# Optimization experiments

Hardware: AMD Instinct MI355X
Metric: run time of the kernel (lower is better)

The kernel has to match this reference:

```python
import jax, jax.numpy as jnp
import numpy as np


def _ln(x, g, b):
    m = x.mean(-1, keepdims=True)
    v = ((x - m) ** 2).mean(-1, keepdims=True)
    return (x - m) * jax.lax.rsqrt(v + 1e-5) * g + b


def _forward(x, fx_in, pre_w1, pre_b1, pre_w2, pre_b2, placeholder,
             ln1_g, ln1_b, px_w, px_b, pfx_w, pfx_b, slice_w, slice_b, temp,
             q_w, k_w, v_w, out_w, out_b, ln2_g, ln2_b,
             mlp_w1, mlp_b1, mlp_w2, mlp_b2,
             ln3_g, ln3_b, head_w1, head_b1, head_w2, head_b2):
    # All linear weights are stored as [in, out] (pre-transposed vs torch nn.Linear).
    B, N, _ = x.shape
    L, H = temp.shape
    dh = slice_w.shape[1]
    gelu = lambda t: jax.nn.gelu(t, approximate=False)
    # preprocess MLP (n_layers=0, res=False): Linear -> GELU -> Linear
    h = jnp.concatenate([x, fx_in], axis=-1)
    h = gelu(h @ pre_w1 + pre_b1) @ pre_w2 + pre_b2
    h = h + placeholder  # learned [D] offset
    scale = 1.0 / jnp.sqrt(jnp.asarray(dh, h.dtype))
    for i in range(L):  # loop over structurally distinct layers
        y = _ln(h, ln1_g[i], ln1_b[i])
        # project to per-head features: bhnd
        fx_mid = (y @ pfx_w[i] + pfx_b[i]).reshape(B, N, H, dh).transpose(0, 2, 1, 3)
        x_mid = (y @ px_w[i] + px_b[i]).reshape(B, N, H, dh).transpose(0, 2, 1, 3)
        # soft slice assignment over G slices
        logits = jnp.einsum('bhnd,dg->bhng', x_mid, slice_w[i]) + slice_b[i]
        sw = jax.nn.softmax(logits / temp[i][None, :, None, None], axis=-1)  # bhng
        norm = sw.sum(axis=2)  # bhg
        tok = jnp.einsum('bhnd,bhng->bhgd', fx_mid, sw) / (norm + 1e-5)[..., None]
        # attention over G=slice_num tokens
        q = tok @ q_w[i]
        k = tok @ k_w[i]
        v = tok @ v_w[i]
        attn = jax.nn.softmax(jnp.einsum('bhgd,bhmd->bhgm', q, k) * scale, axis=-1)
        out_slice = jnp.einsum('bhgm,bhmd->bhgd', attn, v)
        # deslice back to points
        out_x = jnp.einsum('bhgd,bhng->bhnd', out_slice, sw)
        out_x = out_x.transpose(0, 2, 1, 3).reshape(B, N, H * dh)
        h = h + (out_x @ out_w[i] + out_b[i])
        z = _ln(h, ln2_g[i], ln2_b[i])
        h = h + (gelu(z @ mlp_w1[i] + mlp_b1[i]) @ mlp_w2[i] + mlp_b2[i])
    z = _ln(h, ln3_g, ln3_b)
    return gelu(z @ head_w1 + head_b1) @ head_w2 + head_b2


def setup_inputs() -> dict:
    key = jax.random.key(0)
    B, N, D, H, dh, G, L = 2, 16384, 256, 8, 32, 64, 5
    SP, FUN, OUT = 2, 4, 4
    ID = H * dh  # inner_dim == n_hidden
    MR = D * 1   # mlp_ratio=1
    ks = iter(jax.random.split(key, 64))
    nrm = lambda shape, s=0.02: jax.random.normal(next(ks), shape, jnp.float32) * s
    return dict(
        x=jax.random.normal(next(ks), (B, N, SP), jnp.float32),
        fx_in=jax.random.normal(next(ks), (B, N, FUN), jnp.float32),
        pre_w1=nrm((SP + FUN, 2 * D)), pre_b1=jnp.zeros((2 * D,), jnp.float32),
        pre_w2=nrm((2 * D, D)), pre_b2=jnp.zeros((D,), jnp.float32),
        placeholder=nrm((D,)),
        ln1_g=jnp.ones((L, D), jnp.float32), ln1_b=jnp.zeros((L, D), jnp.float32),
        px_w=nrm((L, D, ID)), px_b=jnp.zeros((L, ID), jnp.float32),
        pfx_w=nrm((L, D, ID)), pfx_b=jnp.zeros((L, ID), jnp.float32),
        slice_w=nrm((L, dh, G), 0.1), slice_b=jnp.zeros((L, G), jnp.float32),
        temp=0.5 * jnp.ones((L, H), jnp.float32),
        q_w=nrm((L, dh, dh), 0.1), k_w=nrm((L, dh, dh), 0.1), v_w=nrm((L, dh, dh), 0.1),
        out_w=nrm((L, ID, D)), out_b=jnp.zeros((L, D), jnp.float32),
        ln2_g=jnp.ones((L, D), jnp.float32), ln2_b=jnp.zeros((L, D), jnp.float32),
        mlp_w1=nrm((L, D, MR)), mlp_b1=jnp.zeros((L, MR), jnp.float32),
        mlp_w2=nrm((L, MR, D)), mlp_b2=jnp.zeros((L, D), jnp.float32),
        ln3_g=jnp.ones((D,), jnp.float32), ln3_b=jnp.zeros((D,), jnp.float32),
        head_w1=nrm((D, D)), head_b1=jnp.zeros((D,), jnp.float32),
        head_w2=nrm((D, OUT)), head_b2=jnp.zeros((OUT,), jnp.float32),
    )


def reference(x, fx_in, pre_w1, pre_b1, pre_w2, pre_b2, placeholder,
              ln1_g, ln1_b, px_w, px_b, pfx_w, pfx_b, slice_w, slice_b, temp,
              q_w, k_w, v_w, out_w, out_b, ln2_g, ln2_b,
              mlp_w1, mlp_b1, mlp_w2, mlp_b2,
              ln3_g, ln3_b, head_w1, head_b1, head_w2, head_b2):
    return _forward(x, fx_in, pre_w1, pre_b1, pre_w2, pre_b2, placeholder,
                    ln1_g, ln1_b, px_w, px_b, pfx_w, pfx_b, slice_w, slice_b, temp,
                    q_w, k_w, v_w, out_w, out_b, ln2_g, ln2_b,
                    mlp_w1, mlp_b1, mlp_w2, mlp_b2,
                    ln3_g, ln3_b, head_w1, head_b1, head_w2, head_b2)
```

## Files before the change

### kernel.cpp

```cpp
#include <hip/hip_runtime.h>


#define MTOK 32768
#define NB   16384

typedef unsigned short u16;
using short8 = __attribute__((ext_vector_type(8))) short;
using f4     = __attribute__((ext_vector_type(4))) float;

__device__ __forceinline__ float bfu(u16 u) {
    return __uint_as_float(((unsigned)u) << 16);
}
__device__ __forceinline__ u16 f2bf(float f) {
    unsigned u = __float_as_uint(f);
    u += 0x7FFFu + ((u >> 16) & 1u);
    return (u16)(u >> 16);
}
__device__ __forceinline__ float ldf(const void* p, int i, int isbf) {
    return isbf ? bfu(((const u16*)p)[i]) : ((const float*)p)[i];
}
__device__ __forceinline__ float4 dec4(ushort4 u) {
    return make_float4(bfu(u.x), bfu(u.y), bfu(u.z), bfu(u.w));
}
__device__ __forceinline__ float gelu_f(float x) {
    return 0.5f * x * (1.0f + erff(x * 0.7071067811865475f));
}

typedef __attribute__((address_space(1))) const unsigned int* as1p;
typedef __attribute__((address_space(3))) unsigned int* as3p;
__device__ __forceinline__ void gload_lds16(const u16* g, u16* l) {
    __builtin_amdgcn_global_load_lds((as1p)g, (as3p)l, 16, 0, 0);
}

#define F_H      ((size_t)0)
#define F_OS     ((size_t)8388608)
#define F_TOKP   ((size_t)8421376)
#define F_NORMP  ((size_t)10518528)
#define F_TOK    ((size_t)10584064)
#define F_NORM   ((size_t)10616832)
#define F_BIAS   ((size_t)10617856)
#define F_PARAMS ((size_t)10626048)
#define F_BF     ((size_t)10858884)
#define B_PB2C 0
#define B_OUTB 256
#define B_M1B  1536
#define B_M2B  2816
#define B_HB1  4096
#define B_SP   4352
#define B_END  8192
#define U_WT     ((size_t)0)
#define WT_PRE2  0
#define WT_HEAD1 131072
#define WT_SPFX  196608
#define WT_OUT   1179648
#define WT_MLP1  1507328
#define WT_MLP2  1835008
#define WT_END   2162688
#define U_Y   ((size_t)2162688)
#define U_XM  ((size_t)10551296)
#define U_FM  ((size_t)18939904)
#define U_SW  ((size_t)27328512)

#define P_X    0
#define P_FX   65536
#define P_W1   196608
#define P_B1   199680
#define P_LN1G 200192
#define P_LN1B 201472
#define P_LN2G 202752
#define P_LN2B 204032
#define P_LN3G 205312
#define P_LN3B 205568
#define P_SLW  205824
#define P_SLB  216064
#define P_TEMP 216384
#define P_QW   216448
#define P_KW   221568
#define P_VW   226688
#define P_HW2  231808
#define P_HB2  232832
#define P_END  232836

__global__ __launch_bounds__(256) void cvt_kernel(
    const void* x, const void* fx, const void* w1, const void* b1,
    const void* l1g, const void* l1b, const void* l2g, const void* l2b,
    const void* l3g, const void* l3b, const void* slw, const void* slb,
    const void* tmp, const void* qw, const void* kw, const void* vw,
    const void* hw2, const void* hb2, float* __restrict__ P)
{
    int isbf = (((const u16*)tmp)[0] != 0);
    int idx = blockIdx.x * 256 + threadIdx.x;
    const void* s; int o;
    if      (idx < 65536)  { s = x;   o = idx; }
    else if (idx < 196608) { s = fx;  o = idx - 65536; }
    else if (idx < 199680) { s = w1;  o = idx - 196608; }
    else if (idx < 200192) { s = b1;  o = idx - 199680; }
    else if (idx < 201472) { s = l1g; o = idx - 200192; }
    else if (idx < 202752) { s = l1b; o = idx - 201472; }
    else if (idx < 204032) { s = l2g; o = idx - 202752; }
    else if (idx < 205312) { s = l2b; o = idx - 204032; }
    else if (idx < 205568) { s = l3g; o = idx - 205312; }
    else if (idx < 205824) { s = l3b; o = idx - 205568; }
    else if (idx < 216064) { s = slw; o = idx - 205824; }
    else if (idx < 216384) { s = slb; o = idx - 216064; }
    else if (idx < 216424) { s = tmp; o = idx - 216384; }
    else if (idx < 216448) { return; }
    else if (idx < 221568) { s = qw;  o = idx - 216448; }
    else if (idx < 226688) { s = kw;  o = idx - 221568; }
    else if (idx < 231808) { s = vw;  o = idx - 226688; }
    else if (idx < 232832) { s = hw2; o = idx - 231808; }
    else if (idx < 232836) { s = hb2; o = idx - 232832; }
    else return;
    P[idx] = ldf(s, o, isbf);
}

__global__ __launch_bounds__(256) void prep_main(
    const void* pre_w2, const void* head_w1, const void* pfx_w,
    const void* out_w, const void* mlp_w1, const void* mlp_w2,
    const void* pre_b2, const void* placeholder, const void* pfx_b,
    const void* out_b, const void* mlp_b1, const void* mlp_b2,
    const void* head_b1, const void* tmp,
    u16* __restrict__ WT, float* __restrict__ BIAS)
{
    int isbf = (((const u16*)tmp)[0] != 0);
    int blk = blockIdx.x;
    int t = threadIdx.x;
    if (blk < 368) {
        __shared__ float tile[64][65];
        const void* src; size_t srcoff; size_t dbase; int dstride;
        int k0, n0;
        if (blk < 32) {
            int tk = blk >> 2, tn = blk & 3;
            src = pre_w2; srcoff = 0;
            k0 = tk * 64; n0 = tn * 64;
            dbase = WT_PRE2; dstride = 512;
        } else {
            int m = (blk - 32) >> 4, tl = (blk - 32) & 15;
            int tk = tl >> 2, tn = tl & 3;
            k0 = tk * 64; n0 = tn * 64; dstride = 256;
            if (m == 0)       { src = head_w1; srcoff = 0;               dbase = WT_HEAD1; }
            else if (m <= 5)  { int i = m - 1;  src = pfx_w;  srcoff = (size_t)i * 65536;
                                dbase = WT_SPFX + (size_t)i * 196608 + (size_t)512 * 256; }
            else if (m <= 10) { int i = m - 6;  src = out_w;  srcoff = (size_t)i * 65536;
                                dbase = WT_OUT + (size_t)i * 65536; }
            else if (m <= 15) { int i = m - 11; src = mlp_w1; srcoff = (size_t)i * 65536;
                                dbase = WT_MLP1 + (size_t)i * 65536; }
            else              { int i = m - 16; src = mlp_w2; srcoff = (size_t)i * 65536;
                                dbase = WT_MLP2 + (size_t)i * 65536; }
        }
#pragma unroll
        for (int p = 0; p < 16; ++p) {
            int flat = t + 256 * p;
            int r = flat >> 6, c = flat & 63;
            tile[r][c] = ldf(src, srcoff + (size_t)(k0 + r) * 256 + n0 + c, isbf);
        }
        __syncthreads();
#pragma unroll
        for (int p = 0; p < 16; ++p) {
            int flat = t + 256 * p;
            int r = flat >> 6, c = flat & 63;
            WT[dbase + (size_t)(n0 + r) * dstride + k0 + c] = f2bf(tile[c][r]);
        }
    } else {
        int idx = (blk - 368) * 256 + t;
        if (idx < 256) {
            BIAS[B_PB2C + idx] = ldf(pre_b2, idx, isbf) + ldf(placeholder, idx, isbf);
        } else if (idx < 1536) {
            int o = idx - 256;  BIAS[B_OUTB + o] = ldf(out_b, o, isbf);
        } else if (idx < 2816) {
            int o = idx - 1536; BIAS[B_M1B + o] = ldf(mlp_b1, o, isbf);
        } else if (idx < 4096) {
            int o = idx - 2816; BIAS[B_M2B + o] = ldf(mlp_b2, o, isbf);
        } else if (idx < 4352) {
            int o = idx - 4096; BIAS[B_HB1 + o] = ldf(head_b1, o, isbf);
        } else if (idx < 5632) {
            int o = idx - 4352;
            int i = o >> 8, c = o & 255;
            BIAS[B_SP + i * 768 + 512 + c] = ldf(pfx_b, o, isbf);
        }
    }
}

__global__ __launch_bounds__(256) void prep_pxsl(
    const void* px_w, const void* px_b, const void* slw, const void* slb,
    const void* tmp, u16* __restrict__ WT, float* __restrict__ BIAS)
{
    int isbf = (((const u16*)tmp)[0] != 0);
    __shared__ float pxs[64 * 33];
    __shared__ float sls[2048];
    int blk = blockIdx.x;
    int i = blk >> 5, h = (blk >> 2) & 7, kb = blk & 3;
    int t = threadIdx.x;
#pragma unroll
    for (int p = 0; p < 8; ++p) {
        int flat = t + 256 * p;
        sls[flat] = ldf(slw, i * 2048 + flat, isbf);
        int k = flat >> 5, d = flat & 31;
        pxs[k * 33 + d] = ldf(px_w, i * 65536 + (kb * 64 + k) * 256 + h * 32 + d, isbf);
    }
    __syncthreads();
    int k = t & 63, gb = t >> 6;
    float acc[16];
#pragma unroll
    for (int gi = 0; gi < 16; ++gi) acc[gi] = 0.f;
#pragma unroll
    for (int d = 0; d < 32; ++d) {
        float pv = pxs[k * 33 + d];
        const float* sp = sls + d * 64 + gb * 16;
#pragma unroll
        for (int gi = 0; gi < 16; ++gi) acc[gi] = fmaf(pv, sp[gi], acc[gi]);
    }
    u16* WTp = WT + WT_SPFX + (size_t)i * 196608;
#pragma unroll
    for (int gi = 0; gi < 16; ++gi) {
        int n = h * 64 + gb * 16 + gi;
        WTp[n * 256 + kb * 64 + k] = f2bf(acc[gi]);
    }
    if (kb == 0 && t < 64) {
        int g = t;
        float a = ldf(slb, i * 64 + g, isbf);
#pragma unroll
        for (int d = 0; d < 32; ++d)
            a = fmaf(ldf(px_b, i * 256 + h * 32 + d, isbf), sls[d * 64 + g], a);
        BIAS[B_SP + i * 768 + h * 64 + g] = a;
    }
}

__global__ __launch_bounds__(256) void pre1_kernel(
    const float* __restrict__ P, u16* __restrict__ HID)
{
    __shared__ float w1s[3072];
    __shared__ float b1s[512];
    int t = threadIdx.x;
#pragma unroll
    for (int p = 0; p < 12; ++p) w1s[t + 256 * p] = P[P_W1 + t + 256 * p];
    b1s[t] = P[P_B1 + t];
    b1s[t + 256] = P[P_B1 + t + 256];
    __syncthreads();
    int m = blockIdx.x * 4 + (t >> 6);
    int lane = t & 63;
    float xa = P[P_X + m * 2],      xb = P[P_X + m * 2 + 1];
    float fa = P[P_FX + m * 4],     fb = P[P_FX + m * 4 + 1];
    float fc = P[P_FX + m * 4 + 2], fd = P[P_FX + m * 4 + 3];
    size_t base = (size_t)m * 512 + lane;
#pragma unroll
    for (int jj = 0; jj < 8; ++jj) {
        int j = lane + 64 * jj;
        float a = b1s[j];
        a = fmaf(xa, w1s[j], a);
        a = fmaf(xb, w1s[512 + j], a);
        a = fmaf(fa, w1s[1024 + j], a);
        a = fmaf(fb, w1s[1536 + j], a);
        a = fmaf(fc, w1s[2048 + j], a);
        a = fmaf(fd, w1s[2560 + j], a);
        HID[base + 64 * jj] = f2bf(gelu_f(a));
    }
}

template <int KK, bool RES>
__global__ __launch_bounds__(256, 3) void gemm_ln(
    const u16* __restrict__ A, const u16* __restrict__ Wt,
    const float* __restrict__ bias, const float* __restrict__ lng,
    const float* __restrict__ lnb, u16* __restrict__ Hb, u16* __restrict__ Y)
{
    __shared__ u16 As[64 * 64];
    __shared__ u16 Bs[256 * 64];
    __shared__ float rs2[2][64], rq2[2][64];
    const int t = threadIdx.x;
    const int wave = t >> 6, lane = t & 63;
    const int quad = lane >> 4, l15 = lane & 15;
    const int m0 = blockIdx.x * 64;
    const int wm = (wave & 1) * 32, wn = (wave >> 1) * 128;
    const int lrow = lane >> 3, ls = lane & 7;
    f4 acc[2][8];
#pragma unroll
    for (int i = 0; i < 2; ++i)
#pragma unroll
        for (int j = 0; j < 8; ++j) acc[i][j] = (f4){0.f, 0.f, 0.f, 0.f};

    for (int kc = 0; kc < KK; kc += 64) {
        if (kc) __syncthreads();
#pragma unroll
        for (int q = 0; q < 10; ++q) {
            int gr = wave * 80 + q * 8;
            if (gr < 64) {
                int row = gr + lrow;
                int chunk = ls ^ lrow;
                gload_lds16(A + (size_t)(m0 + row) * KK + kc + chunk * 8,
                            As + gr * 64);
            } else {
                int brow = gr - 64 + lrow;
                int chunk = ls ^ lrow;
                gload_lds16(Wt + (size_t)brow * KK + kc + chunk * 8,
                            Bs + (gr - 64) * 64);
            }
        }
        __syncthreads();
#pragma unroll
        for (int kk = 0; kk < 2; ++kk) {
            short8 a[2], b[8];
#pragma unroll
            for (int i = 0; i < 2; ++i) {
                int R = wm + i * 16 + l15;
                a[i] = *(const short8*)(As + R * 64 + (((quad + kk * 4) ^ (R & 7)) << 3));
            }
#pragma unroll
            for (int j = 0; j < 8; ++j) {
// ... 132 lines not shown
            }
    }
#pragma unroll
    for (int i = 0; i < 2; ++i)
#pragma unroll
        for (int j = 0; j < 8; ++j) acc[i][j] = (f4){0.f, 0.f, 0.f, 0.f};

    for (int kc = 0; kc < 256; kc += 64) {
        __syncthreads();
#pragma unroll
        for (int q = 0; q < 8; ++q) {
            int gr = wave * 64 + q * 8;
            int brow = gr + lrow;
            gload_lds16(W2 + (size_t)brow * 256 + kc + (ls ^ lrow) * 8,
                        Bs + gr * 64);
        }
        __syncthreads();
#pragma unroll
        for (int kk = 0; kk < 2; ++kk) {
            short8 a[2], b[8];
#pragma unroll
            for (int i = 0; i < 2; ++i) {
                int R = wm + i * 16 + l15;
                a[i] = *(const short8*)(hs + R * 264 + kc + kk * 32 + quad * 8);
            }
#pragma unroll
            for (int j = 0; j < 8; ++j) {
                int Rb = wn + j * 16 + l15;
                b[j] = *(const short8*)(Bs + Rb * 64 + (((quad + kk * 4) ^ (Rb & 7)) << 3));
            }
#pragma unroll
            for (int i = 0; i < 2; ++i)
#pragma unroll
                for (int j = 0; j < 8; ++j)
                    acc[i][j] = __builtin_amdgcn_mfma_f32_16x16x32_bf16(
                        a[i], b[j], acc[i][j], 0, 0, 0);
        }
    }
    float bj[8];
#pragma unroll
    for (int j = 0; j < 8; ++j) bj[j] = b2[colj[j]];
    const int half = wn >> 7;
#pragma unroll
    for (int i = 0; i < 2; ++i) {
#pragma unroll
        for (int r = 0; r < 4; ++r) {
            int row = wm + i * 16 + quad * 4 + r;
            size_t gbase = (size_t)(m0 + row) * 256;
            float s = 0.f, q2 = 0.f;
#pragma unroll
            for (int j = 0; j < 8; ++j) {
                float v = acc[i][j][r] + bj[j] + bfu(Hb[gbase + colj[j]]);
                Hb[gbase + colj[j]] = f2bf(v);
                acc[i][j][r] = v;
                s += v; q2 += v * v;
            }
#pragma unroll
            for (int o = 1; o < 16; o <<= 1) { s += __shfl_xor(s, o); q2 += __shfl_xor(q2, o); }
            if (l15 == 0) { rs2[half][row] = s; rq2[half][row] = q2; }
        }
    }
    __syncthreads();
    float gj[8], betj[8];
#pragma unroll
    for (int j = 0; j < 8; ++j) { gj[j] = lng[colj[j]]; betj[j] = lnb[colj[j]]; }
#pragma unroll
    for (int i = 0; i < 2; ++i) {
#pragma unroll
        for (int r = 0; r < 4; ++r) {
            int row = wm + i * 16 + quad * 4 + r;
            size_t gbase = (size_t)(m0 + row) * 256;
            float mean = (rs2[0][row] + rs2[1][row]) * (1.0f / 256.0f);
            float var = (rq2[0][row] + rq2[1][row]) * (1.0f / 256.0f) - mean * mean;
            float rstd = rsqrtf(var + 1e-5f);
#pragma unroll
            for (int j = 0; j < 8; ++j) {
                float y = (acc[i][j][r] - mean) * rstd * gj[j] + betj[j];
                Y[gbase + colj[j]] = f2bf(y);
            }
        }
    }
}

__global__ __launch_bounds__(256, 4) void gemm_gelu(
    const u16* __restrict__ A, const u16* __restrict__ Wt,
    const float* __restrict__ bias, u16* __restrict__ Cb)
{
    __shared__ u16 As[128 * 64];
    __shared__ u16 Bs[128 * 64];
    const int t = threadIdx.x;
    const int wave = t >> 6, lane = t & 63;
    const int quad = lane >> 4, l15 = lane & 15;
    const int m0 = blockIdx.x * 128;
    const int n0 = blockIdx.y * 128;
    const int wm = (wave & 1) * 64, wn = (wave >> 1) * 64;
    const int r0 = wave * 32;
    const int lrow = lane >> 3, ls = lane & 7;
    f4 acc[4][4];
#pragma unroll
    for (int i = 0; i < 4; ++i)
#pragma unroll
        for (int j = 0; j < 4; ++j) acc[i][j] = (f4){0.f, 0.f, 0.f, 0.f};

    for (int kc = 0; kc < 256; kc += 64) {
        if (kc) __syncthreads();
#pragma unroll
        for (int q = 0; q < 4; ++q) {
            int row = r0 + q * 8 + lrow;
            int chunk = ls ^ (row & 7);
            gload_lds16(A  + (size_t)(m0 + row) * 256 + kc + chunk * 8,
                        As + (r0 + q * 8) * 64);
            gload_lds16(Wt + (size_t)(n0 + row) * 256 + kc + chunk * 8,
                        Bs + (r0 + q * 8) * 64);
        }
        __syncthreads();
#pragma unroll
        for (int kk = 0; kk < 2; ++kk) {
            short8 a[4], b[4];
#pragma unroll
            for (int i = 0; i < 4; ++i) {
                int R = wm + i * 16 + l15;
                a[i] = *(const short8*)(As + R * 64 + (((quad + kk * 4) ^ (R & 7)) << 3));
            }
#pragma unroll
            for (int j = 0; j < 4; ++j) {
                int R = wn + j * 16 + l15;
                b[j] = *(const short8*)(Bs + R * 64 + (((quad + kk * 4) ^ (R & 7)) << 3));
            }
#pragma unroll
            for (int i = 0; i < 4; ++i)
#pragma unroll
                for (int j = 0; j < 4; ++j)
                    acc[i][j] = __builtin_amdgcn_mfma_f32_16x16x32_bf16(
                        a[i], b[j], acc[i][j], 0, 0, 0);
        }
    }
#pragma unroll
    for (int j = 0; j < 4; ++j) {
        int cj = n0 + wn + j * 16 + l15;
        float bj = bias[cj];
#pragma unroll
        for (int i = 0; i < 4; ++i) {
            int rbase = m0 + wm + i * 16 + quad * 4;
#pragma unroll
            for (int r = 0; r < 4; ++r) {
                float v = gelu_f(acc[i][j][r] + bj);
                Cb[(size_t)(rbase + r) * 256 + cj] = f2bf(v);
            }
        }
    }
}

__global__ __launch_bounds__(256, 4) void gemm_spfx(
    const u16* __restrict__ A, const u16* __restrict__ Wt,
    const float* __restrict__ bsp, const float* __restrict__ tempv,
    u16* __restrict__ SW, u16* __restrict__ FM)
{
    __shared__ u16 As[128 * 64];
    __shared__ u16 Bs[128 * 64];
    const int t = threadIdx.x;
    const int wave = t >> 6, lane = t & 63;
    const int quad = lane >> 4, l15 = lane & 15;
    const int m0 = blockIdx.x * 128;
    const int n0 = blockIdx.y * 128;
    const int wm = (wave & 1) * 64, wn = (wave >> 1) * 64;
    const int r0 = wave * 32;
    const int lrow = lane >> 3, ls = lane & 7;
    f4 acc[4][4];
#pragma unroll
    for (int i = 0; i < 4; ++i)
#pragma unroll
        for (int j = 0; j < 4; ++j) acc[i][j] = (f4){0.f, 0.f, 0.f, 0.f};

    for (int kc = 0; kc < 256; kc += 64) {
        if (kc) __syncthreads();
#pragma unroll
        for (int q = 0; q < 4; ++q) {
            int row = r0 + q * 8 + lrow;
            int chunk = ls ^ (row & 7);
            gload_lds16(A  + (size_t)(m0 + row) * 256 + kc + chunk * 8,
                        As + (r0 + q * 8) * 64);
            gload_lds16(Wt + (size_t)(n0 + row) * 256 + kc + chunk * 8,
                        Bs + (r0 + q * 8) * 64);
        }
        __syncthreads();
#pragma unroll
        for (int kk = 0; kk < 2; ++kk) {
            short8 a[4], b[4];
#pragma unroll
            for (int i = 0; i < 4; ++i) {
                int R = wm + i * 16 + l15;
                a[i] = *(const short8*)(As + R * 64 + (((quad + kk * 4) ^ (R & 7)) << 3));
            }
#pragma unroll
            for (int j = 0; j < 4; ++j) {
                int R = wn + j * 16 + l15;
                b[j] = *(const short8*)(Bs + R * 64 + (((quad + kk * 4) ^ (R & 7)) << 3));
            }
#pragma unroll
            for (int i = 0; i < 4; ++i)
#pragma unroll
                for (int j = 0; j < 4; ++j)
                    acc[i][j] = __builtin_amdgcn_mfma_f32_16x16x32_bf16(
                        a[i], b[j], acc[i][j], 0, 0, 0);
        }
    }
    float bj[4];
#pragma unroll
    for (int j = 0; j < 4; ++j) bj[j] = bsp[n0 + wn + j * 16 + l15];
    if (blockIdx.y < 4) {
        const int h = (n0 + wn) >> 6;
        const float itemp = 1.0f / tempv[h];
#pragma unroll
        for (int i = 0; i < 4; ++i) {
#pragma unroll
            for (int r = 0; r < 4; ++r) {
                float v[4];
                float mx = -3.0e38f;
#pragma unroll
                for (int j = 0; j < 4; ++j) {
                    v[j] = (acc[i][j][r] + bj[j]) * itemp;
                    mx = fmaxf(mx, v[j]);
                }
#pragma unroll
                for (int o = 1; o < 16; o <<= 1) mx = fmaxf(mx, __shfl_xor(mx, o));
                float s = 0.f;
#pragma unroll
                for (int j = 0; j < 4; ++j) { v[j] = expf(v[j] - mx); s += v[j]; }
#pragma unroll
                for (int o = 1; o < 16; o <<= 1) s += __shfl_xor(s, o);
                float inv = 1.0f / s;
                int m = m0 + wm + i * 16 + quad * 4 + r;
                int b = m >> 14, n = m & 16383;
// ... 142 lines not shown
            float4 kv = kr[e4];
            s = fmaf(qv[e4].x, kv.x, s); s = fmaf(qv[e4].y, kv.y, s);
            s = fmaf(qv[e4].z, kv.z, s); s = fmaf(qv[e4].w, kv.w, s);
        }
        s *= 0.17677669529663687f;
        p[mm] = s;
        mx = fmaxf(mx, s);
    }
    mx = fmaxf(mx, __shfl_xor(mx, 1));
    mx = fmaxf(mx, __shfl_xor(mx, 2));
    float lsum = 0.f;
#pragma unroll
    for (int mm = 0; mm < 16; ++mm) { p[mm] = expf(p[mm] - mx); lsum += p[mm]; }
    lsum += __shfl_xor(lsum, 1);
    lsum += __shfl_xor(lsum, 2);
    float inv = 1.0f / lsum;
    float4 oa[8];
#pragma unroll
    for (int d4 = 0; d4 < 8; ++d4) oa[d4] = make_float4(0.f, 0.f, 0.f, 0.f);
#pragma unroll
    for (int mm = 0; mm < 16; ++mm) {
        int mI = sub * 16 + mm;
        const float4* vr = (const float4*)(vs + mI * 32);
        float pm = p[mm];
#pragma unroll
        for (int d4 = 0; d4 < 8; ++d4) {
            float4 vv = vr[d4];
            oa[d4].x = fmaf(pm, vv.x, oa[d4].x);
            oa[d4].y = fmaf(pm, vv.y, oa[d4].y);
            oa[d4].z = fmaf(pm, vv.z, oa[d4].z);
            oa[d4].w = fmaf(pm, vv.w, oa[d4].w);
        }
    }
#pragma unroll
    for (int d4 = 0; d4 < 8; ++d4) {
        oa[d4].x += __shfl_xor(oa[d4].x, 1); oa[d4].x += __shfl_xor(oa[d4].x, 2);
        oa[d4].y += __shfl_xor(oa[d4].y, 1); oa[d4].y += __shfl_xor(oa[d4].y, 2);
        oa[d4].z += __shfl_xor(oa[d4].z, 1); oa[d4].z += __shfl_xor(oa[d4].z, 2);
        oa[d4].w += __shfl_xor(oa[d4].w, 1); oa[d4].w += __shfl_xor(oa[d4].w, 2);
    }
    float4 r0 = oa[sub * 2], r1 = oa[sub * 2 + 1];
    r0.x *= inv; r0.y *= inv; r0.z *= inv; r0.w *= inv;
    r1.x *= inv; r1.y *= inv; r1.z *= inv; r1.w *= inv;
    *(float4*)(OS + (size_t)bh * 2048 + g * 32 + sub * 8)     = r0;
    *(float4*)(OS + (size_t)bh * 2048 + g * 32 + sub * 8 + 4) = r1;
}

__global__ __launch_bounds__(256) void deslice_kernel(
    const float* __restrict__ OS, const u16* __restrict__ SW, u16* __restrict__ OX)
{
    __shared__ float swt[8 * 16 * 64];
    int blk = blockIdx.x;
    int b = blk >> 10, n0 = (blk & 1023) * 16;
    int t = threadIdx.x;
    int hd = t >> 5, d = t & 31;
#pragma unroll
    for (int i = 0; i < 8; ++i) {
        int f4v = t + 256 * i;
        int hd2 = f4v >> 8, mm = (f4v >> 4) & 15, g4 = f4v & 15;
        ushort4 u = *(const ushort4*)(SW + (((size_t)(b * 8 + hd2)) * NB + n0 + mm) * 64 + g4 * 4);
        *(float4*)&swt[(hd2 * 16 + mm) * 64 + g4 * 4] = dec4(u);
    }
    __syncthreads();
    float acc[16];
#pragma unroll
    for (int mm = 0; mm < 16; ++mm) acc[mm] = 0.f;
    const float* osb = OS + ((size_t)(b * 8 + hd)) * 2048 + d;
#pragma unroll 4
    for (int g4 = 0; g4 < 16; ++g4) {
        float o0 = osb[(g4 * 4 + 0) * 32], o1 = osb[(g4 * 4 + 1) * 32];
        float o2 = osb[(g4 * 4 + 2) * 32], o3 = osb[(g4 * 4 + 3) * 32];
        const float* swp = swt + hd * 1024 + g4 * 4;
#pragma unroll
        for (int mm = 0; mm < 16; ++mm) {
            float4 sv = *(const float4*)(swp + mm * 64);
            acc[mm] = fmaf(o0, sv.x, fmaf(o1, sv.y, fmaf(o2, sv.z, fmaf(o3, sv.w, acc[mm]))));
        }
    }
#pragma unroll
    for (int mm = 0; mm < 16; ++mm)
        OX[((size_t)b * NB + n0 + mm) * 256 + t] = f2bf(acc[mm]);
}

__global__ __launch_bounds__(256) void head2_kernel(
    const u16* __restrict__ HID, const float* __restrict__ w2,
    const float* __restrict__ b2, const void* tmp, void* __restrict__ OUT)
{
    int isbf = (((const u16*)tmp)[0] != 0);
    int lane = threadIdx.x & 63;
    size_t m = (size_t)blockIdx.x * 4 + (threadIdx.x >> 6);
    const float4 hv = dec4(*(const ushort4*)(HID + m * 256 + lane * 4));
    float4 a = make_float4(0.f, 0.f, 0.f, 0.f);
    float hcomp[4] = {hv.x, hv.y, hv.z, hv.w};
#pragma unroll
    for (int i = 0; i < 4; ++i) {
        const float4 wv = *(const float4*)(w2 + (lane * 4 + i) * 4);
        float h = hcomp[i];
        a.x = fmaf(h, wv.x, a.x); a.y = fmaf(h, wv.y, a.y);
        a.z = fmaf(h, wv.z, a.z); a.w = fmaf(h, wv.w, a.w);
    }
#pragma unroll
    for (int o = 32; o; o >>= 1) {
        a.x += __shfl_xor(a.x, o); a.y += __shfl_xor(a.y, o);
        a.z += __shfl_xor(a.z, o); a.w += __shfl_xor(a.w, o);
    }
    if (lane == 0) {
        float o0 = a.x + b2[0], o1 = a.y + b2[1], o2 = a.z + b2[2], o3 = a.w + b2[3];
        if (isbf) {
            ushort4 r; r.x = f2bf(o0); r.y = f2bf(o1); r.z = f2bf(o2); r.w = f2bf(o3);
            *(ushort4*)((u16*)OUT + m * 4) = r;
        } else {
            *(float4*)((float*)OUT + m * 4) = make_float4(o0, o1, o2, o3);
        }
    }
}

extern "C" void kernel_launch(void* const* d_in, const int* in_sizes, int n_in,
                              void* d_out, int out_size, void* d_ws, size_t ws_size,
                              hipStream_t stream)
{
    const void* x = d_in[0];      const void* fx = d_in[1];
    const void* pre_w1 = d_in[2]; const void* pre_b1 = d_in[3];
    const void* pre_w2 = d_in[4]; const void* pre_b2 = d_in[5];
    const void* placeholder = d_in[6];
    const void* ln1_g = d_in[7];  const void* ln1_b = d_in[8];
    const void* px_w = d_in[9];   const void* px_b = d_in[10];
    const void* pfx_w = d_in[11]; const void* pfx_b = d_in[12];
    const void* slice_w = d_in[13]; const void* slice_b = d_in[14];
    const void* temp = d_in[15];
    const void* q_w = d_in[16];   const void* k_w = d_in[17]; const void* v_w = d_in[18];
    const void* out_w = d_in[19]; const void* out_b = d_in[20];
    const void* ln2_g = d_in[21]; const void* ln2_b = d_in[22];
    const void* mlp_w1 = d_in[23]; const void* mlp_b1 = d_in[24];
    const void* mlp_w2 = d_in[25]; const void* mlp_b2 = d_in[26];
    const void* ln3_g = d_in[27]; const void* ln3_b = d_in[28];
    const void* head_w1 = d_in[29]; const void* head_b1 = d_in[30];
    const void* head_w2 = d_in[31]; const void* head_b2 = d_in[32];

    float* ws = (float*)d_ws;
    u16*   Hb    = (u16*)(ws + F_H);
    float* OSp   = ws + F_OS;
    float* TOKP  = ws + F_TOKP;
    float* NORMP = ws + F_NORMP;
    float* TOKf  = ws + F_TOK;
    float* NORMf = ws + F_NORM;
    float* BIAS  = ws + F_BIAS;
    float* P     = ws + F_PARAMS;
    u16*   U     = (u16*)(ws + F_BF);
    u16*   WT    = U + U_WT;
    u16*   Yb    = U + U_Y;
    u16*   XMb   = U + U_XM;
    u16*   FMb   = U + U_FM;
    u16*   SWb   = U + U_SW;
    u16*   HIDb  = U + U_XM;

    cvt_kernel<<<910, 256, 0, stream>>>(x, fx, pre_w1, pre_b1, ln1_g, ln1_b,
        ln2_g, ln2_b, ln3_g, ln3_b, slice_w, slice_b, temp, q_w, k_w, v_w,
        head_w2, head_b2, P);
    prep_main<<<390, 256, 0, stream>>>(pre_w2, head_w1, pfx_w, out_w, mlp_w1,
        mlp_w2, pre_b2, placeholder, pfx_b, out_b, mlp_b1, mlp_b2, head_b1,
        temp, WT, BIAS);
    prep_pxsl<<<160, 256, 0, stream>>>(px_w, px_b, slice_w, slice_b, temp, WT, BIAS);
    pre1_kernel<<<8192, 256, 0, stream>>>(P, HIDb);

    dim3 gpl(256, 2);
    dim3 gsp(256, 6);
    gemm_ln<512, false><<<512, 256, 0, stream>>>(HIDb, WT + WT_PRE2,
        BIAS + B_PB2C, P + P_LN1G, P + P_LN1B, Hb, Yb);

    for (int i = 0; i < 5; ++i) {
        gemm_spfx<<<gsp, 256, 0, stream>>>(Yb, WT + WT_SPFX + (size_t)i * 196608,
            BIAS + B_SP + i * 768, P + P_TEMP + i * 8, SWb, FMb);
        tok1_kernel<<<1024, 256, 0, stream>>>(FMb, SWb, TOKP, NORMP);
        tok2_kernel<<<132, 256, 0, stream>>>(TOKP, NORMP, TOKf, NORMf);
        attn_kernel<<<16, 256, 0, stream>>>(TOKf, NORMf, P + P_QW + i * 1024,
            P + P_KW + i * 1024, P + P_VW + i * 1024, OSp);
        deslice_kernel<<<2048, 256, 0, stream>>>(OSp, SWb, Yb);
        gemm_ln<256, true><<<512, 256, 0, stream>>>(Yb, WT + WT_OUT + i * 65536,
            BIAS + B_OUTB + i * 256, P + P_LN2G + i * 256, P + P_LN2B + i * 256, Hb, Yb);
        const float* ng = (i < 4) ? (P + P_LN1G + (i + 1) * 256) : (P + P_LN3G);
        const float* nb = (i < 4) ? (P + P_LN1B + (i + 1) * 256) : (P + P_LN3B);
        gemm_mlp<<<512, 256, 0, stream>>>(Yb, WT + WT_MLP1 + i * 65536,
            BIAS + B_M1B + i * 256, WT + WT_MLP2 + i * 65536,
            BIAS + B_M2B + i * 256, ng, nb, Hb, Yb);
    }

    gemm_gelu<<<gpl, 256, 0, stream>>>(Yb, WT + WT_HEAD1, BIAS + B_HB1, XMb);
    head2_kernel<<<8192, 256, 0, stream>>>(XMb, P + P_HW2, P + P_HB2, temp, d_out);
}
```

Measured before the change: 1.047 ms.

## Merge prep kernels into one launch and fuse head GEMM with output projection

Folds the three parameter-preparation kernels into a single launch that dispatches on block index, cutting two launches. Replaces the head GELU GEMM plus the separate head2 reduction kernel with one kernel. Each block computes a 64x256 GELU hidden tile, keeps it in shared memory, and applies the 256x4 output projection directly. This removes the hidden-activation round trip through global memory and one launch, at the cost of heavier shared-memory use per block (~58KB) and a scalar tail loop for the final projection.

```diff
diff --git a/kernel.cpp b/kernel.cpp
--- a/kernel.cpp
+++ b/kernel.cpp
@@ -81,148 +81,140 @@
 #define P_HB2  232832
 #define P_END  232836
 
-__global__ __launch_bounds__(256) void cvt_kernel(
+__global__ __launch_bounds__(256) void prep_all(
     const void* x, const void* fx, const void* w1, const void* b1,
     const void* l1g, const void* l1b, const void* l2g, const void* l2b,
     const void* l3g, const void* l3b, const void* slw, const void* slb,
     const void* tmp, const void* qw, const void* kw, const void* vw,
-    const void* hw2, const void* hb2, float* __restrict__ P)
-{
-    int isbf = (((const u16*)tmp)[0] != 0);
-    int idx = blockIdx.x * 256 + threadIdx.x;
-    const void* s; int o;
-    if      (idx < 65536)  { s = x;   o = idx; }
-    else if (idx < 196608) { s = fx;  o = idx - 65536; }
-    else if (idx < 199680) { s = w1;  o = idx - 196608; }
-    else if (idx < 200192) { s = b1;  o = idx - 199680; }
-    else if (idx < 201472) { s = l1g; o = idx - 200192; }
-    else if (idx < 202752) { s = l1b; o = idx - 201472; }
-    else if (idx < 204032) { s = l2g; o = idx - 202752; }
-    else if (idx < 205312) { s = l2b; o = idx - 204032; }
-    else if (idx < 205568) { s = l3g; o = idx - 205312; }
-    else if (idx < 205824) { s = l3b; o = idx - 205568; }
-    else if (idx < 216064) { s = slw; o = idx - 205824; }
-    else if (idx < 216384) { s = slb; o = idx - 216064; }
-    else if (idx < 216424) { s = tmp; o = idx - 216384; }
-    else if (idx < 216448) { return; }
-    else if (idx < 221568) { s = qw;  o = idx - 216448; }
-    else if (idx < 226688) { s = kw;  o = idx - 221568; }
-    else if (idx < 231808) { s = vw;  o = idx - 226688; }
-    else if (idx < 232832) { s = hw2; o = idx - 231808; }
-    else if (idx < 232836) { s = hb2; o = idx - 232832; }
-    else return;
-    P[idx] = ldf(s, o, isbf);
-}
-
-__global__ __launch_bounds__(256) void prep_main(
-    const void* pre_w2, const void* head_w1, const void* pfx_w,
-    const void* out_w, const void* mlp_w1, const void* mlp_w2,
+    const void* hw2, const void* hb2,
+    const void* pre_w2, const void* head_w1, const void* px_w, const void* px_b,
+    const void* pfx_w, const void* out_w, const void* mlp_w1, const void* mlp_w2,
     const void* pre_b2, const void* placeholder, const void* pfx_b,
-    const void* out_b, const void* mlp_b1, const void* mlp_b2,
-    const void* head_b1, const void* tmp,
-    u16* __restrict__ WT, float* __restrict__ BIAS)
-{
+    const void* out_b, const void* mlp_b1, const void* mlp_b2, const void* head_b1,
+    float* __restrict__ P, u16* __restrict__ WT, float* __restrict__ BIAS)
+{
+    __shared__ float shbuf[64 * 65];
     int isbf = (((const u16*)tmp)[0] != 0);
     int blk = blockIdx.x;
     int t = threadIdx.x;
-    if (blk < 368) {
-        __shared__ float tile[64][65];
-        const void* src; size_t srcoff; size_t dbase; int dstride;
-        int k0, n0;
-        if (blk < 32) {
-            int tk = blk >> 2, tn = blk & 3;
-            src = pre_w2; srcoff = 0;
-            k0 = tk * 64; n0 = tn * 64;
-            dbase = WT_PRE2; dstride = 512;
+    if (blk < 910) {
+        int idx = blk * 256 + t;
+        const void* s; int o;
+        if      (idx < 65536)  { s = x;   o = idx; }
+        else if (idx < 196608) { s = fx;  o = idx - 65536; }
+        else if (idx < 199680) { s = w1;  o = idx - 196608; }
+        else if (idx < 200192) { s = b1;  o = idx - 199680; }
+        else if (idx < 201472) { s = l1g; o = idx - 200192; }
+        else if (idx < 202752) { s = l1b; o = idx - 201472; }
+        else if (idx < 204032) { s = l2g; o = idx - 202752; }
+        else if (idx < 205312) { s = l2b; o = idx - 204032; }
+        else if (idx < 205568) { s = l3g; o = idx - 205312; }
+        else if (idx < 205824) { s = l3b; o = idx - 205568; }
+        else if (idx < 216064) { s = slw; o = idx - 205824; }
+        else if (idx < 216384) { s = slb; o = idx - 216064; }
+        else if (idx < 216424) { s = tmp; o = idx - 216384; }
+        else if (idx < 216448) { return; }
+        else if (idx < 221568) { s = qw;  o = idx - 216448; }
+        else if (idx < 226688) { s = kw;  o = idx - 221568; }
+        else if (idx < 231808) { s = vw;  o = idx - 226688; }
+        else if (idx < 232832) { s = hw2; o = idx - 231808; }
+        else if (idx < 232836) { s = hb2; o = idx - 232832; }
+        else return;
+        P[idx] = ldf(s, o, isbf);
+    } else if (blk < 1300) {
+        int bb = blk - 910;
+        if (bb < 368) {
+            float (*tile)[65] = (float(*)[65])shbuf;
+            const void* src; size_t srcoff; size_t dbase; int dstride;
+            int k0, n0;
+            if (bb < 32) {
+                int tk = bb >> 2, tn = bb & 3;
+                src = pre_w2; srcoff = 0;
+                k0 = tk * 64; n0 = tn * 64;
+                dbase = WT_PRE2; dstride = 512;
+            } else {
+                int m = (bb - 32) >> 4, tl = (bb - 32) & 15;
+                int tk = tl >> 2, tn = tl & 3;
+                k0 = tk * 64; n0 = tn * 64; dstride = 256;
+                if (m == 0)       { src = head_w1; srcoff = 0;               dbase = WT_HEAD1; }
+                else if (m <= 5)  { int i = m - 1;  src = pfx_w;  srcoff = (size_t)i * 65536;
+                                    dbase = WT_SPFX + (size_t)i * 196608 + (size_t)512 * 256; }
+                else if (m <= 10) { int i = m - 6;  src = out_w;  srcoff = (size_t)i * 65536;
+                                    dbase = WT_OUT + (size_t)i * 65536; }
+                else if (m <= 15) { int i = m - 11; src = mlp_w1; srcoff = (size_t)i * 65536;
+                                    dbase = WT_MLP1 + (size_t)i * 65536; }
+                else              { int i = m - 16; src = mlp_w2; srcoff = (size_t)i * 65536;
+                                    dbase = WT_MLP2 + (size_t)i * 65536; }
+            }
+#pragma unroll
+            for (int p = 0; p < 16; ++p) {
+                int flat = t + 256 * p;
+                int r = flat >> 6, c = flat & 63;
+                tile[r][c] = ldf(src, srcoff + (size_t)(k0 + r) * 256 + n0 + c, isbf);
+            }
+            __syncthreads();
+#pragma unroll
+            for (int p = 0; p < 16; ++p) {
+                int flat = t + 256 * p;
+                int r = flat >> 6, c = flat & 63;
+                WT[dbase + (size_t)(n0 + r) * dstride + k0 + c] = f2bf(tile[c][r]);
+            }
         } else {
-            int m = (blk - 32) >> 4, tl = (blk - 32) & 15;
-            int tk = tl >> 2, tn = tl & 3;
-            k0 = tk * 64; n0 = tn * 64; dstride = 256;
-            if (m == 0)       { src = head_w1; srcoff = 0;               dbase = WT_HEAD1; }
-            else if (m <= 5)  { int i = m - 1;  src = pfx_w;  srcoff = (size_t)i * 65536;
-                                dbase = WT_SPFX + (size_t)i * 196608 + (size_t)512 * 256; }
-            else if (m <= 10) { int i = m - 6;  src = out_w;  srcoff = (size_t)i * 65536;
-                                dbase = WT_OUT + (size_t)i * 65536; }
-            else if (m <= 15) { int i = m - 11; src = mlp_w1; srcoff = (size_t)i * 65536;
-                                dbase = WT_MLP1 + (size_t)i * 65536; }
-            else              { int i = m - 16; src = mlp_w2; srcoff = (size_t)i * 65536;
-                                dbase = WT_MLP2 + (size_t)i * 65536; }
-        }
-#pragma unroll
-        for (int p = 0; p < 16; ++p) {
+            int idx = (bb - 368) * 256 + t;
+            if (idx < 256) {
+                BIAS[B_PB2C + idx] = ldf(pre_b2, idx, isbf) + ldf(placeholder, idx, isbf);
+            } else if (idx < 1536) {
+                int o = idx - 256;  BIAS[B_OUTB + o] = ldf(out_b, o, isbf);
+            } else if (idx < 2816) {
+                int o = idx - 1536; BIAS[B_M1B + o] = ldf(mlp_b1, o, isbf);
+            } else if (idx < 4096) {
+                int o = idx - 2816; BIAS[B_M2B + o] = ldf(mlp_b2, o, isbf);
+            } else if (idx < 4352) {
+                int o = idx - 4096; BIAS[B_HB1 + o] = ldf(head_b1, o, isbf);
+            } else if (idx < 5632) {
+                int o = idx - 4352;
+                int i = o >> 8, c = o & 255;
+                BIAS[B_SP + i * 768 + 512 + c] = ldf(pfx_b, o, isbf);
+            }
+        }
+    } else {
+        float* pxs = shbuf;
+        float* sls = shbuf + 2112;
+        int bb = blk - 1300;
+        int i = bb >> 5, h = (bb >> 2) & 7, kb = bb & 3;
+#pragma unroll
+        for (int p = 0; p < 8; ++p) {
             int flat = t + 256 * p;
-            int r = flat >> 6, c = flat & 63;
-            tile[r][c] = ldf(src, srcoff + (size_t)(k0 + r) * 256 + n0 + c, isbf);
+            sls[flat] = ldf(slw, i * 2048 + flat, isbf);
+            int k = flat >> 5, d = flat & 31;
+            pxs[k * 33 + d] = ldf(px_w, i * 65536 + (kb * 64 + k) * 256 + h * 32 + d, isbf);
         }
         __syncthreads();
-#pragma unroll
-        for (int p = 0; p < 16; ++p) {
-            int flat = t + 256 * p;
-            int r = flat >> 6, c = flat & 63;
-            WT[dbase + (size_t)(n0 + r) * dstride + k0 + c] = f2bf(tile[c][r]);
-        }
-    } else {
-        int idx = (blk - 368) * 256 + t;
-        if (idx < 256) {
-            BIAS[B_PB2C + idx] = ldf(pre_b2, idx, isbf) + ldf(placeholder, idx, isbf);
-        } else if (idx < 1536) {
-            int o = idx - 256;  BIAS[B_OUTB + o] = ldf(out_b, o, isbf);
-        } else if (idx < 2816) {
-            int o = idx - 1536; BIAS[B_M1B + o] = ldf(mlp_b1, o, isbf);
-        } else if (idx < 4096) {
-            int o = idx - 2816; BIAS[B_M2B + o] = ldf(mlp_b2, o, isbf);
-        } else if (idx < 4352) {
-            int o = idx - 4096; BIAS[B_HB1 + o] = ldf(head_b1, o, isbf);
-        } else if (idx < 5632) {
-            int o = idx - 4352;
-            int i = o >> 8, c = o & 255;
-            BIAS[B_SP + i * 768 + 512 + c] = ldf(pfx_b, o, isbf);
-        }
-    }
-}
-
-__global__ __launch_bounds__(256) void prep_pxsl(
-    const void* px_w, const void* px_b, const void* slw, const void* slb,
-    const void* tmp, u16* __restrict__ WT, float* __restrict__ BIAS)
-{
-    int isbf = (((const u16*)tmp)[0] != 0);
-    __shared__ float pxs[64 * 33];
-    __shared__ float sls[2048];
-    int blk = blockIdx.x;
-    int i = blk >> 5, h = (blk >> 2) & 7, kb = blk & 3;
-    int t = threadIdx.x;
-#pragma unroll
-    for (int p = 0; p < 8; ++p) {
-        int flat = t + 256 * p;
-        sls[flat] = ldf(slw, i * 2048 + flat, isbf);
-        int k = flat >> 5, d = flat & 31;
-        pxs[k * 33 + d] = ldf(px_w, i * 65536 + (kb * 64 + k) * 256 + h * 32 + d, isbf);
-    }
-    __syncthreads();
-    int k = t & 63, gb = t >> 6;
-    float acc[16];
-#pragma unroll
-    for (int gi = 0; gi < 16; ++gi) acc[gi] = 0.f;
-#pragma unroll
-    for (int d = 0; d < 32; ++d) {
-        float pv = pxs[k * 33 + d];
-        const float* sp = sls + d * 64 + gb * 16;
-#pragma unroll
-        for (int gi = 0; gi < 16; ++gi) acc[gi] = fmaf(pv, sp[gi], acc[gi]);
-    }
-    u16* WTp = WT + WT_SPFX + (size_t)i * 196608;
-#pragma unroll
-    for (int gi = 0; gi < 16; ++gi) {
-        int n = h * 64 + gb * 16 + gi;
-        WTp[n * 256 + kb * 64 + k] = f2bf(acc[gi]);
-    }
-    if (kb == 0 && t < 64) {
-        int g = t;
-        float a = ldf(slb, i * 64 + g, isbf);
-#pragma unroll
-        for (int d = 0; d < 32; ++d)
-            a = fmaf(ldf(px_b, i * 256 + h * 32 + d, isbf), sls[d * 64 + g], a);
-        BIAS[B_SP + i * 768 + h * 64 + g] = a;
+        int k = t & 63, gb = t >> 6;
+        float acc[16];
+#pragma unroll
+        for (int gi = 0; gi < 16; ++gi) acc[gi] = 0.f;
+#pragma unroll
+        for (int d = 0; d < 32; ++d) {
+            float pv = pxs[k * 33 + d];
+            const float* sp = sls + d * 64 + gb * 16;
+#pragma unroll
+            for (int gi = 0; gi < 16; ++gi) acc[gi] = fmaf(pv, sp[gi], acc[gi]);
+        }
+        u16* WTp = WT + WT_SPFX + (size_t)i * 196608;
+#pragma unroll
+        for (int gi = 0; gi < 16; ++gi) {
+            int n = h * 64 + gb * 16 + gi;
+            WTp[n * 256 + kb * 64 + k] = f2bf(acc[gi]);
+        }
+        if (kb == 0 && t < 64) {
+            int g = t;
+            float a = ldf(slb, i * 64 + g, isbf);
+#pragma unroll
+            for (int d = 0; d < 32; ++d)
+                a = fmaf(ldf(px_b, i * 256 + h * 32 + d, isbf), sls[d * 64 + g], a);
+            BIAS[B_SP + i * 768 + h * 64 + g] = a;
+        }
     }
 }
 
@@ -521,73 +513,93 @@
     }
 }
 
-__global__ __launch_bounds__(256, 4) void gemm_gelu(
-    const u16* __restrict__ A, const u16* __restrict__ Wt,
-    const float* __restrict__ bias, u16* __restrict__ Cb)
-{
-    __shared__ u16 As[128 * 64];
-    __shared__ u16 Bs[128 * 64];
+__global__ __launch_bounds__(256, 2) void gemm_head(
+    const u16* __restrict__ A, const u16* __restrict__ W1,
+    const float* __restrict__ b1, const float* __restrict__ P,
+    const void* tmp, void* __restrict__ OUT)
+{
+    __shared__ u16 As[64 * 64];
+    __shared__ u16 Bs[256 * 64];
+    __shared__ u16 hs[64 * 264];
+    __shared__ float w2s[1024];
     const int t = threadIdx.x;
     const int wave = t >> 6, lane = t & 63;
     const int quad = lane >> 4, l15 = lane & 15;
-    const int m0 = blockIdx.x * 128;
-    const int n0 = blockIdx.y * 128;
-    const int wm = (wave & 1) * 64, wn = (wave >> 1) * 64;
-    const int r0 = wave * 32;
+    const int m0 = blockIdx.x * 64;
+    const int wm = (wave & 1) * 32, wn = (wave >> 1) * 128;
     const int lrow = lane >> 3, ls = lane & 7;
-    f4 acc[4][4];
-#pragma unroll
-    for (int i = 0; i < 4; ++i)
-#pragma unroll
-        for (int j = 0; j < 4; ++j) acc[i][j] = (f4){0.f, 0.f, 0.f, 0.f};
+#pragma unroll
+    for (int p = 0; p < 4; ++p) w2s[t + 256 * p] = P[P_HW2 + t + 256 * p];
+    f4 acc[2][8];
+#pragma unroll
+    for (int i = 0; i < 2; ++i)
+#pragma unroll
+        for (int j = 0; j < 8; ++j) acc[i][j] = (f4){0.f, 0.f, 0.f, 0.f};
 
     for (int kc = 0; kc < 256; kc += 64) {
         if (kc) __syncthreads();
 #pragma unroll
-        for (int q = 0; q < 4; ++q) {
-            int row = r0 + q * 8 + lrow;
-            int chunk = ls ^ (row & 7);
-            gload_lds16(A  + (size_t)(m0 + row) * 256 + kc + chunk * 8,
-                        As + (r0 + q * 8) * 64);
-            gload_lds16(Wt + (size_t)(n0 + row) * 256 + kc + chunk * 8,
-                        Bs + (r0 + q * 8) * 64);
+        for (int q = 0; q < 10; ++q) {
+            int gr = wave * 80 + q * 8;
+            if (gr < 64) {
+                int row = gr + lrow;
+                gload_lds16(A + (size_t)(m0 + row) * 256 + kc + (ls ^ lrow) * 8,
+                            As + gr * 64);
+            } else {
+                int brow = gr - 64 + lrow;
+                gload_lds16(W1 + (size_t)brow * 256 + kc + (ls ^ lrow) * 8,
+                            Bs + (gr - 64) * 64);
+            }
         }
         __syncthreads();
 #pragma unroll
         for (int kk = 0; kk < 2; ++kk) {
-            short8 a[4], b[4];
-#pragma unroll
-            for (int i = 0; i < 4; ++i) {
+            short8 a[2], b[8];
+#pragma unroll
+            for (int i = 0; i < 2; ++i) {
                 int R = wm + i * 16 + l15;
                 a[i] = *(const short8*)(As + R * 64 + (((quad + kk * 4) ^ (R & 7)) << 3));
             }
 #pragma unroll
-            for (int j = 0; j < 4; ++j) {
-                int R = wn + j * 16 + l15;
-                b[j] = *(const short8*)(Bs + R * 64 + (((quad + kk * 4) ^ (R & 7)) << 3));
-            }
-#pragma unroll
-            for (int i = 0; i < 4; ++i)
-#pragma unroll
-                for (int j = 0; j < 4; ++j)
+            for (int j = 0; j < 8; ++j) {
+                int Rb = wn + j * 16 + l15;
+                b[j] = *(const short8*)(Bs + Rb * 64 + (((quad + kk * 4) ^ (Rb & 7)) << 3));
+            }
+#pragma unroll
+            for (int i = 0; i < 2; ++i)
+#pragma unroll
+                for (int j = 0; j < 8; ++j)
                     acc[i][j] = __builtin_amdgcn_mfma_f32_16x16x32_bf16(
                         a[i], b[j], acc[i][j], 0, 0, 0);
         }
     }
-#pragma unroll
-    for (int j = 0; j < 4; ++j) {
-        int cj = n0 + wn + j * 16 + l15;
-        float bj = bias[cj];
-#pragma unroll
-        for (int i = 0; i < 4; ++i) {
-            int rbase = m0 + wm + i * 16 + quad * 4;
+    {
+        float bj[8];
+        int colj[8];
+#pragma unroll
+        for (int j = 0; j < 8; ++j) { colj[j] = wn + j * 16 + l15; bj[j] = b1[colj[j]]; }
+#pragma unroll
+        for (int i = 0; i < 2; ++i)
 #pragma unroll
             for (int r = 0; r < 4; ++r) {
-                float v = gelu_f(acc[i][j][r] + bj);
-                Cb[(size_t)(rbase + r) * 256 + cj] = f2bf(v);
-            }
-        }
-    }
+                int row = wm + i * 16 + quad * 4 + r;
+#pragma unroll
+                for (int j = 0; j < 8; ++j)
+                    hs[row * 264 + colj[j]] = f2bf(gelu_f(acc[i][j][r] + bj[j]));
+            }
+    }
+    __syncthreads();
+    int isbf = (((const u16*)tmp)[0] != 0);
+    int row = t >> 2, c = t & 3;
+    const u16* hrow = hs + row * 264;
+    float a = 0.f;
+#pragma unroll 8
+    for (int k = 0; k < 256; ++k)
+        a = fmaf(bfu(hrow[k]), w2s[k * 4 + c], a);
+    a += P[P_HB2 + c];
+    size_t off = (size_t)(m0 + row) * 4 + c;
+    if (isbf) ((u16*)OUT)[off] = f2bf(a);
+    else      ((float*)OUT)[off] = a;
 }
 
 __global__ __launch_bounds__(256, 4) void gemm_spfx(
@@ -896,39 +908,6 @@
         OX[((size_t)b * NB + n0 + mm) * 256 + t] = f2bf(acc[mm]);
 }
 
-__global__ __launch_bounds__(256) void head2_kernel(
-    const u16* __restrict__ HID, const float* __restrict__ w2,
-    const float* __restrict__ b2, const void* tmp, void* __restrict__ OUT)
-{
-    int isbf = (((const u16*)tmp)[0] != 0);
-    int lane = threadIdx.x & 63;
-    size_t m = (size_t)blockIdx.x * 4 + (threadIdx.x >> 6);
-    const float4 hv = dec4(*(const ushort4*)(HID + m * 256 + lane * 4));
-    float4 a = make_float4(0.f, 0.f, 0.f, 0.f);
-    float hcomp[4] = {hv.x, hv.y, hv.z, hv.w};
-#pragma unroll
-    for (int i = 0; i < 4; ++i) {
-        const float4 wv = *(const float4*)(w2 + (lane * 4 + i) * 4);
-        float h = hcomp[i];
-        a.x = fmaf(h, wv.x, a.x); a.y = fmaf(h, wv.y, a.y);
-        a.z = fmaf(h, wv.z, a.z); a.w = fmaf(h, wv.w, a.w);
-    }
-#pragma unroll
-    for (int o = 32; o; o >>= 1) {
-        a.x += __shfl_xor(a.x, o); a.y += __shfl_xor(a.y, o);
-        a.z += __shfl_xor(a.z, o); a.w += __shfl_xor(a.w, o);
-    }
-    if (lane == 0) {
-        float o0 = a.x + b2[0], o1 = a.y + b2[1], o2 = a.z + b2[2], o3 = a.w + b2[3];
-        if (isbf) {
-            ushort4 r; r.x = f2bf(o0); r.y = f2bf(o1); r.z = f2bf(o2); r.w = f2bf(o3);
-            *(ushort4*)((u16*)OUT + m * 4) = r;
-        } else {
-            *(float4*)((float*)OUT + m * 4) = make_float4(o0, o1, o2, o3);
-        }
-    }
-}
-
 extern "C" void kernel_launch(void* const* d_in, const int* in_sizes, int n_in,
                               void* d_out, int out_size, void* d_ws, size_t ws_size,
                               hipStream_t stream)
@@ -963,21 +942,18 @@
     u16*   U     = (u16*)(ws + F_BF);
     u16*   WT    = U + U_WT;
     u16*   Yb    = U + U_Y;
-    u16*   XMb   = U + U_XM;
     u16*   FMb   = U + U_FM;
     u16*   SWb   = U + U_SW;
     u16*   HIDb  = U + U_XM;
 
-    cvt_kernel<<<910, 256, 0, stream>>>(x, fx, pre_w1, pre_b1, ln1_g, ln1_b,
+    prep_all<<<1460, 256, 0, stream>>>(x, fx, pre_w1, pre_b1, ln1_g, ln1_b,
         ln2_g, ln2_b, ln3_g, ln3_b, slice_w, slice_b, temp, q_w, k_w, v_w,
-        head_w2, head_b2, P);
-    prep_main<<<390, 256, 0, stream>>>(pre_w2, head_w1, pfx_w, out_w, mlp_w1,
-        mlp_w2, pre_b2, placeholder, pfx_b, out_b, mlp_b1, mlp_b2, head_b1,
-        temp, WT, BIAS);
-    prep_pxsl<<<160, 256, 0, stream>>>(px_w, px_b, slice_w, slice_b, temp, WT, BIAS);
+        head_w2, head_b2,
+        pre_w2, head_w1, px_w, px_b, pfx_w, out_w, mlp_w1, mlp_w2,
+        pre_b2, placeholder, pfx_b, out_b, mlp_b1, mlp_b2, head_b1,
+        P, WT, BIAS);
     pre1_kernel<<<8192, 256, 0, stream>>>(P, HIDb);
 
-    dim3 gpl(256, 2);
     dim3 gsp(256, 6);
     gemm_ln<512, false><<<512, 256, 0, stream>>>(HIDb, WT + WT_PRE2,
         BIAS + B_PB2C, P + P_LN1G, P + P_LN1B, Hb, Yb);
@@ -999,6 +975,6 @@
             BIAS + B_M2B + i * 256, ng, nb, Hb, Yb);
     }
 
-    gemm_gelu<<<gpl, 256, 0, stream>>>(Yb, WT + WT_HEAD1, BIAS + B_HB1, XMb);
-    head2_kernel<<<8192, 256, 0, stream>>>(XMb, P + P_HW2, P + P_HB2, temp, d_out);
-}
+    gemm_head<<<512, 256, 0, stream>>>(Yb, WT + WT_HEAD1, BIAS + B_HB1,
+        P, temp, d_out);
+}
```

After: 1.030 ms. No clear change (-1.7%).
